# Kernel tuning notes

Measured on AMD Instinct MI355X. Metric: run time of the kernel, lower is better.

The kernel has to match this reference:

```python
import jax, jax.numpy as jnp
import numpy as np

B = 65536  # number of 32-bit words processed by the VM


def _build_tables():
    # ByteToNibbleFFN: byte one-hot -> (high, low) nibble one-hots
    W1_b2n = np.eye(256, dtype=np.float32)
    W2_b2n = np.zeros((256, 32), dtype=np.float32)
    for b in range(256):
        W2_b2n[b, (b >> 4) & 15] = 1.0
        W2_b2n[b, 16 + (b & 15)] = 1.0
    # NibbleToByteFFN: (high, low) -> byte one-hot
    W1_n2b = np.zeros((32, 256), dtype=np.float32)
    for high in range(16):
        for low in range(16):
            bv = (high << 4) | low
            W1_n2b[high, bv] = 1.0
            W1_n2b[16 + low, bv] = 1.0
    W2_n2b = np.eye(256, dtype=np.float32)
    # NibbleTableFFN for XOR
    W1_xor = np.zeros((32, 256), dtype=np.float32)
    W2_xor = np.zeros((256, 16), dtype=np.float32)
    for a in range(16):
        for b in range(16):
            k = a * 16 + b
            W1_xor[a, k] = 1.0
            W1_xor[16 + b, k] = 1.0
            W2_xor[k, (a ^ b) & 15] = 1.0
    # NibbleAddFFN: (a, b, carry) -> (sum, carry)
    W1_add = np.zeros((34, 512), dtype=np.float32)
    W2_sum = np.zeros((512, 16), dtype=np.float32)
    W2_carry = np.zeros((512, 2), dtype=np.float32)
    for a in range(16):
        for b in range(16):
            for c in range(2):
                k = a * 32 + b * 2 + c
                W1_add[a, k] = 1.0
                W1_add[16 + b, k] = 1.0
                W1_add[32 + c, k] = 1.0
                total = a + b + c
                W2_sum[k, total & 15] = 1.0
                W2_carry[k, 1 if total >= 16 else 0] = 1.0
    return (jnp.asarray(W1_b2n), jnp.asarray(W2_b2n), jnp.asarray(W1_n2b),
            jnp.asarray(W2_n2b), jnp.asarray(W1_xor), jnp.asarray(W2_xor),
            jnp.asarray(W1_add), jnp.asarray(W2_sum), jnp.asarray(W2_carry))


def setup_inputs() -> dict:
    key = jax.random.key(0)
    k1, k2 = jax.random.split(key)
    a_idx = jax.random.randint(k1, (B, 4), 0, 256)
    b_idx = jax.random.randint(k2, (B, 4), 0, 256)
    a_bytes = jax.nn.one_hot(a_idx, 256, dtype=jnp.float32)  # [B,4,256]
    b_bytes = jax.nn.one_hot(b_idx, 256, dtype=jnp.float32)
    (W1_b2n, W2_b2n, W1_n2b, W2_n2b, W1_xor, W2_xor,
     W1_add, W2_sum, W2_carry) = _build_tables()
    return {
        'a_bytes': a_bytes, 'b_bytes': b_bytes,
        'W1_b2n': W1_b2n, 'W2_b2n': W2_b2n,
        'W1_n2b': W1_n2b, 'W2_n2b': W2_n2b,
        'W1_xor': W1_xor, 'W2_xor': W2_xor,
        'W1_add': W1_add, 'W2_sum': W2_sum, 'W2_carry': W2_carry,
    }


def reference(a_bytes, b_bytes, W1_b2n, W2_b2n, W1_n2b, W2_n2b,
              W1_xor, W2_xor, W1_add, W2_sum, W2_carry):
    # Batched faithful translation of the torch VM: the torch code loops over
    # single words; here each op is vectorized over the word batch B while the
    # fixed 4-byte carry chain remains an explicit (structural) loop.
    def byte_to_nib(x):                       # x: [B,256]
        w = jax.nn.softmax((x @ W1_b2n) * 100.0, axis=-1)
        nib = w @ W2_b2n                      # [B,32]
        return nib[:, :16], nib[:, 16:]

    def nib_to_byte(high, low):               # [B,16] each -> [B,256]
        x = jnp.concatenate([high, low], axis=-1)
        w = jax.nn.softmax((x @ W1_n2b - 1.5) * 20.0, axis=-1)
        return w @ W2_n2b

    def nib_xor(a, b):                        # [B,16] each -> [B,16]
        x = jnp.concatenate([a, b], axis=-1)
        w = jax.nn.softmax((x @ W1_xor - 1.5) * 20.0, axis=-1)
        return w @ W2_xor

    def nib_add(a, b, c):                     # [B,16],[B,16],[B,2]
        x = jnp.concatenate([a, b, c], axis=-1)
        w = jax.nn.softmax((x @ W1_add - 2.5) * 20.0, axis=-1)
        return w @ W2_sum, w @ W2_carry

    def byte_xor(a, b):                       # [B,256] each
        a_h, a_l = byte_to_nib(a)
        b_h, b_l = byte_to_nib(b)
        return nib_to_byte(nib_xor(a_h, b_h), nib_xor(a_l, b_l))

    n = a_bytes.shape[0]
    # ByteAddFFN: 4-byte ripple-carry add, carry starts as one-hot 0
    carry = jnp.broadcast_to(jnp.array([1.0, 0.0], dtype=a_bytes.dtype), (n, 2))
    sum_bytes = []
    for i in range(4):
        a_h, a_l = byte_to_nib(a_bytes[:, i])
        b_h, b_l = byte_to_nib(b_bytes[:, i])
        r_low, carry_low = nib_add(a_l, b_l, carry)
        r_high, carry = nib_add(a_h, b_h, carry_low)
        sum_bytes.append(nib_to_byte(r_high, r_low))
    # Chain a second VM op: XOR the sum with operand a, per byte
    out = [byte_xor(sum_bytes[i], a_bytes[:, i]) for i in range(4)]
    return jnp.stack(out, axis=1)             # [B,4,256]
```

## Files before the change

kernel.cpp:

```cpp
#include <hip/hip_runtime.h>
#include <stdint.h>


typedef float f32x4 __attribute__((ext_vector_type(4)));

__device__ __forceinline__ uint32_t row_index(f32x4 v) {
    const bool nx = v.x != 0.0f, ny = v.y != 0.0f, nz = v.z != 0.0f, nw = v.w != 0.0f;
    const unsigned long long m  = __ballot(nx | ny | nz | nw);
    const unsigned long long m0 = __ballot(ny | nw);
    const unsigned long long m1 = __ballot(nz | nw);
    const int src = __ffsll(m) - 1;
    return ((uint32_t)src << 2) |
           (uint32_t)((m0 >> src) & 1ull) |
           ((uint32_t)((m1 >> src) & 1ull) << 1);
}

__device__ __forceinline__ f32x4 onehot4(int j, uint32_t oi) {
    f32x4 r;
    r.x = ((uint32_t)j     == oi) ? 1.0f : 0.0f;
    r.y = ((uint32_t)j + 1 == oi) ? 1.0f : 0.0f;
    r.z = ((uint32_t)j + 2 == oi) ? 1.0f : 0.0f;
    r.w = ((uint32_t)j + 3 == oi) ? 1.0f : 0.0f;
    return r;
}

__global__ __launch_bounds__(256) void vm_kernel(
    const f32x4* __restrict__ a4,
    const f32x4* __restrict__ b4,
    f32x4* __restrict__ o4,
    int n_words)
{
    const int word = (blockIdx.x << 2) | (threadIdx.x >> 6);
    const int lane = threadIdx.x & 63;
    if (word >= n_words) return;

    const long base = (long)word * 256 + lane;

    const f32x4 av0 = a4[base];       const f32x4 av1 = a4[base + 64];
    const f32x4 av2 = a4[base + 128]; const f32x4 av3 = a4[base + 192];
    const f32x4 bv0 = b4[base];       const f32x4 bv1 = b4[base + 64];
    const f32x4 bv2 = b4[base + 128]; const f32x4 bv3 = b4[base + 192];

    const uint32_t aw = row_index(av0)        | (row_index(av1) << 8) |
                        (row_index(av2) << 16) | (row_index(av3) << 24);
    const uint32_t bw = row_index(bv0)        | (row_index(bv1) << 8) |
                        (row_index(bv2) << 16) | (row_index(bv3) << 24);

    const uint32_t s = aw + bw;
    const uint32_t o = s ^ aw;

    const int j = lane * 4;
    __builtin_nontemporal_store(onehot4(j,  o        & 255u), &o4[base]);
    __builtin_nontemporal_store(onehot4(j, (o >> 8)  & 255u), &o4[base + 64]);
    __builtin_nontemporal_store(onehot4(j, (o >> 16) & 255u), &o4[base + 128]);
    __builtin_nontemporal_store(onehot4(j, (o >> 24) & 255u), &o4[base + 192]);
}

extern "C" void kernel_launch(void* const* d_in, const int* in_sizes, int n_in,
                              void* d_out, int out_size, void* d_ws, size_t ws_size,
                              hipStream_t stream)
{
    const f32x4* a4 = (const f32x4*)d_in[0];
    const f32x4* b4 = (const f32x4*)d_in[1];
    f32x4* o4 = (f32x4*)d_out;
    const int n_words = in_sizes[0] / 1024;
    const int n_blocks = (n_words + 3) / 4;
    vm_kernel<<<n_blocks, 256, 0, stream>>>(a4, b4, o4, n_words);
}
```

Measured before the change: 602.2 us.

## Split into read-only index pass and write-only one-hot expansion pass

Splits the fused kernel into two launches. The first reads the one-hot inputs with a grid-stride loop and stores one packed uint32 result per word to workspace. The second expands those indices into one-hot output with plain stores instead of nontemporal ones. The goal is to separate read and write DRAM traffic so neither phase contends with the other, at the cost of an extra launch and a small workspace round trip. The fused path is kept as a fallback and now also uses regular stores.

```diff
diff --git a/kernel.cpp b/kernel.cpp
--- a/kernel.cpp
+++ b/kernel.cpp
@@ -24,36 +24,67 @@
     return r;
 }
 
-__global__ __launch_bounds__(256) void vm_kernel(
-    const f32x4* __restrict__ a4,
-    const f32x4* __restrict__ b4,
-    f32x4* __restrict__ o4,
-    int n_words)
+__global__ __launch_bounds__(256) void pass1_idx(
+    const f32x4* __restrict__ a4, const f32x4* __restrict__ b4,
+    uint32_t* __restrict__ idx, int n_words)
+{
+    const int lane    = threadIdx.x & 63;
+    const int wave    = (blockIdx.x << 2) | (threadIdx.x >> 6);
+    const int n_waves = gridDim.x << 2;
+    for (int word = wave; word < n_words; word += n_waves) {
+        const long base = (long)word * 256 + lane;
+        const f32x4 av0 = a4[base];       const f32x4 bv0 = b4[base];
+        const f32x4 av1 = a4[base + 64];  const f32x4 bv1 = b4[base + 64];
+        const f32x4 av2 = a4[base + 128]; const f32x4 bv2 = b4[base + 128];
+        const f32x4 av3 = a4[base + 192]; const f32x4 bv3 = b4[base + 192];
+        const uint32_t aw = row_index(av0)        | (row_index(av1) << 8) |
+                            (row_index(av2) << 16) | (row_index(av3) << 24);
+        const uint32_t bw = row_index(bv0)        | (row_index(bv1) << 8) |
+                            (row_index(bv2) << 16) | (row_index(bv3) << 24);
+        const uint32_t o = (aw + bw) ^ aw;
+        if (lane == 0) idx[word] = o;
+    }
+}
+
+__global__ __launch_bounds__(256) void pass2_write(
+    const uint32_t* __restrict__ idx, f32x4* __restrict__ o4, int n_words)
+{
+    const int lane    = threadIdx.x & 63;
+    const int wave    = (blockIdx.x << 2) | (threadIdx.x >> 6);
+    const int n_waves = gridDim.x << 2;
+    for (int word = wave; word < n_words; word += n_waves) {
+        const uint32_t o = idx[word];
+        const long base = (long)word * 256 + lane;
+        const int j = lane * 4;
+        o4[base]       = onehot4(j,  o        & 255u);
+        o4[base + 64]  = onehot4(j, (o >> 8)  & 255u);
+        o4[base + 128] = onehot4(j, (o >> 16) & 255u);
+        o4[base + 192] = onehot4(j, (o >> 24) & 255u);
+    }
+}
+
+__global__ __launch_bounds__(256) void vm_fused(
+    const f32x4* __restrict__ a4, const f32x4* __restrict__ b4,
+    f32x4* __restrict__ o4, int n_words)
 {
     const int word = (blockIdx.x << 2) | (threadIdx.x >> 6);
     const int lane = threadIdx.x & 63;
     if (word >= n_words) return;
-
     const long base = (long)word * 256 + lane;
-
     const f32x4 av0 = a4[base];       const f32x4 av1 = a4[base + 64];
     const f32x4 av2 = a4[base + 128]; const f32x4 av3 = a4[base + 192];
     const f32x4 bv0 = b4[base];       const f32x4 bv1 = b4[base + 64];
     const f32x4 bv2 = b4[base + 128]; const f32x4 bv3 = b4[base + 192];
-
     const uint32_t aw = row_index(av0)        | (row_index(av1) << 8) |
                         (row_index(av2) << 16) | (row_index(av3) << 24);
     const uint32_t bw = row_index(bv0)        | (row_index(bv1) << 8) |
                         (row_index(bv2) << 16) | (row_index(bv3) << 24);
-
-    const uint32_t s = aw + bw;
-    const uint32_t o = s ^ aw;
-
+    const uint32_t o = (aw + bw) ^ aw;
     const int j = lane * 4;
-    __builtin_nontemporal_store(onehot4(j,  o        & 255u), &o4[base]);
-    __builtin_nontemporal_store(onehot4(j, (o >> 8)  & 255u), &o4[base + 64]);
-    __builtin_nontemporal_store(onehot4(j, (o >> 16) & 255u), &o4[base + 128]);
-    __builtin_nontemporal_store(onehot4(j, (o >> 24) & 255u), &o4[base + 192]);
+    o4[base]       = onehot4(j,  o        & 255u);
+    o4[base + 64]  = onehot4(j, (o >> 8)  & 255u);
+    o4[base + 128] = onehot4(j, (o >> 16) & 255u);
+    o4[base + 192] = onehot4(j, (o >> 24) & 255u);
 }
 
 extern "C" void kernel_launch(void* const* d_in, const int* in_sizes, int n_in,
@@ -64,6 +95,12 @@
     const f32x4* b4 = (const f32x4*)d_in[1];
     f32x4* o4 = (f32x4*)d_out;
     const int n_words = in_sizes[0] / 1024;
-    const int n_blocks = (n_words + 3) / 4;
-    vm_kernel<<<n_blocks, 256, 0, stream>>>(a4, b4, o4, n_words);
+
+    if (ws_size >= (size_t)n_words * sizeof(uint32_t)) {
+        uint32_t* idx = (uint32_t*)d_ws;
+        pass1_idx <<<1024, 256, 0, stream>>>(a4, b4, idx, n_words);
+        pass2_write<<<4096, 256, 0, stream>>>(idx, o4, n_words);
+    } else {
+        vm_fused<<<(n_words + 3) / 4, 256, 0, stream>>>(a4, b4, o4, n_words);
+    }
 }
```

Measured after the change: 603.7 us. Within noise of the previous version (+0.3%).

## Use persistent grid-stride waves with software-prefetched next word

Applied to the files above, without the earlier changes.

Replaces the one-wave-per-word launch with a fixed grid of 1024 blocks. Each wave loops over words in a grid stride and loads the next word's inputs before computing and storing the current one, so load latency overlaps with stores. Output stores also change from nontemporal to ordinary stores. The kernel is bandwidth-bound, so the payoff depends on whether fewer resident waves with register double-buffering keep enough memory requests in flight. The store change may add cache pollution.

```diff
diff --git a/kernel.cpp b/kernel.cpp
--- a/kernel.cpp
+++ b/kernel.cpp
@@ -24,36 +24,53 @@
     return r;
 }
 
-__global__ __launch_bounds__(256) void vm_kernel(
+__global__ __launch_bounds__(256) void vm_pipe(
     const f32x4* __restrict__ a4,
     const f32x4* __restrict__ b4,
     f32x4* __restrict__ o4,
     int n_words)
 {
-    const int word = (blockIdx.x << 2) | (threadIdx.x >> 6);
-    const int lane = threadIdx.x & 63;
+    const int lane    = threadIdx.x & 63;
+    const int wave    = (blockIdx.x << 2) | (threadIdx.x >> 6);
+    const int n_waves = gridDim.x << 2;
+
+    int word = wave;
     if (word >= n_words) return;
 
-    const long base = (long)word * 256 + lane;
+    long base = (long)word * 256 + lane;
+    f32x4 a0 = a4[base], a1 = a4[base + 64], a2 = a4[base + 128], a3 = a4[base + 192];
+    f32x4 b0 = b4[base], b1 = b4[base + 64], b2 = b4[base + 128], b3 = b4[base + 192];
 
-    const f32x4 av0 = a4[base];       const f32x4 av1 = a4[base + 64];
-    const f32x4 av2 = a4[base + 128]; const f32x4 av3 = a4[base + 192];
-    const f32x4 bv0 = b4[base];       const f32x4 bv1 = b4[base + 64];
-    const f32x4 bv2 = b4[base + 128]; const f32x4 bv3 = b4[base + 192];
+    while (true) {
+        const int  next  = word + n_waves;
+        const bool more  = next < n_words;
+        const long nbase = (long)next * 256 + lane;
 
-    const uint32_t aw = row_index(av0)        | (row_index(av1) << 8) |
-                        (row_index(av2) << 16) | (row_index(av3) << 24);
-    const uint32_t bw = row_index(bv0)        | (row_index(bv1) << 8) |
-                        (row_index(bv2) << 16) | (row_index(bv3) << 24);
+        f32x4 na0, na1, na2, na3, nb0, nb1, nb2, nb3;
+        if (more) {
+            na0 = a4[nbase];       na1 = a4[nbase + 64];
+            na2 = a4[nbase + 128]; na3 = a4[nbase + 192];
+            nb0 = b4[nbase];       nb1 = b4[nbase + 64];
+            nb2 = b4[nbase + 128]; nb3 = b4[nbase + 192];
+        }
 
-    const uint32_t s = aw + bw;
-    const uint32_t o = s ^ aw;
+        const uint32_t aw = row_index(a0)        | (row_index(a1) << 8) |
+                            (row_index(a2) << 16) | (row_index(a3) << 24);
+        const uint32_t bw = row_index(b0)        | (row_index(b1) << 8) |
+                            (row_index(b2) << 16) | (row_index(b3) << 24);
+        const uint32_t o  = (aw + bw) ^ aw;
 
-    const int j = lane * 4;
-    __builtin_nontemporal_store(onehot4(j,  o        & 255u), &o4[base]);
-    __builtin_nontemporal_store(onehot4(j, (o >> 8)  & 255u), &o4[base + 64]);
-    __builtin_nontemporal_store(onehot4(j, (o >> 16) & 255u), &o4[base + 128]);
-    __builtin_nontemporal_store(onehot4(j, (o >> 24) & 255u), &o4[base + 192]);
+        const int j = lane * 4;
+        o4[base]       = onehot4(j,  o        & 255u);
+        o4[base + 64]  = onehot4(j, (o >> 8)  & 255u);
+        o4[base + 128] = onehot4(j, (o >> 16) & 255u);
+        o4[base + 192] = onehot4(j, (o >> 24) & 255u);
+
+        if (!more) break;
+        word = next; base = nbase;
+        a0 = na0; a1 = na1; a2 = na2; a3 = na3;
+        b0 = nb0; b1 = nb1; b2 = nb2; b3 = nb3;
+    }
 }
 
 extern "C" void kernel_launch(void* const* d_in, const int* in_sizes, int n_in,
@@ -64,6 +81,5 @@
     const f32x4* b4 = (const f32x4*)d_in[1];
     f32x4* o4 = (f32x4*)d_out;
     const int n_words = in_sizes[0] / 1024;
-    const int n_blocks = (n_words + 3) / 4;
-    vm_kernel<<<n_blocks, 256, 0, stream>>>(a4, b4, o4, n_words);
+    vm_pipe<<<1024, 256, 0, stream>>>(a4, b4, o4, n_words);
 }
```

Result: no change. 590.6 us (-1.9%).
